# Performance work log

Hardware: AMD Instinct MI355X
Metric: run time of the kernel (lower is better)

Reference implementation:

```python
import jax, jax.numpy as jnp
import numpy as np

LN_EPS = 1e-3

def setup_inputs() -> dict:
    key = jax.random.key(0)
    ks = jax.random.split(key, 3)
    B, H, W, C = 32, 64, 48, 256
    groups = 8
    d = C // groups
    x = jax.random.normal(ks[0], (B, H, W, C), dtype=jnp.float32)
    conv1x1_w = jax.random.normal(ks[1], (d, d), dtype=jnp.float32) * (1.0 / np.sqrt(d))
    conv1x1_b = jnp.zeros((d,), dtype=jnp.float32)
    conv3x3_w = jax.random.normal(ks[2], (3, 3, d, d), dtype=jnp.float32) * (1.0 / np.sqrt(9 * d))
    conv3x3_b = jnp.zeros((d,), dtype=jnp.float32)
    ln_gamma = jnp.ones((d,), dtype=jnp.float32)
    ln_beta = jnp.zeros((d,), dtype=jnp.float32)
    return {"x": x, "conv1x1_w": conv1x1_w, "conv1x1_b": conv1x1_b,
            "conv3x3_w": conv3x3_w, "conv3x3_b": conv3x3_b,
            "ln_gamma": ln_gamma, "ln_beta": ln_beta, "groups": groups}


def reference(x, conv1x1_w, conv1x1_b, conv3x3_w, conv3x3_b, ln_gamma, ln_beta, groups):
    B, H, W, C = x.shape
    g = groups
    d = C // g
    # group split: [B,H,W,C] -> [B*g, H, W, d]
    gx = x.reshape(B, H, W, g, d).transpose(0, 3, 1, 2, 4).reshape(B * g, H, W, d)
    # adaptive pools to (H,1) and (1,W) == mean over W / mean over H
    x_h = gx.mean(axis=2, keepdims=True)                 # [Bg,H,1,d]
    x_w = gx.mean(axis=1, keepdims=True)                 # [Bg,1,W,d]
    hw = jnp.concatenate([x_h, x_w.transpose(0, 2, 1, 3)], axis=1)  # [Bg,H+W,1,d]
    # conv1x1 == per-position linear over channels
    hw = jnp.einsum('bhwd,de->bhwe', hw, conv1x1_w) + conv1x1_b
    xh = jax.nn.sigmoid(hw[:, :H])                       # [Bg,H,1,d]
    xw = jax.nn.sigmoid(hw[:, H:].transpose(0, 2, 1, 3)) # [Bg,1,W,d]
    # LayerNorm over last axis
    y = gx * xh * xw
    mu = y.mean(axis=-1, keepdims=True)
    var = jnp.mean(jnp.square(y - mu), axis=-1, keepdims=True)
    x1 = (y - mu) * jax.lax.rsqrt(var + LN_EPS) * ln_gamma + ln_beta
    # conv3x3 SAME on grouped features
    x2 = jax.lax.conv_general_dilated(
        gx, conv3x3_w, window_strides=(1, 1), padding='SAME',
        dimension_numbers=('NHWC', 'HWIO', 'NHWC')) + conv3x3_b
    # channel softmax of GAP, cross matmuls -> spatial gate
    x11 = jax.nn.softmax(x1.mean(axis=(1, 2)), axis=-1)  # [Bg,d]
    x21 = jax.nn.softmax(x2.mean(axis=(1, 2)), axis=-1)  # [Bg,d]
    w1 = jnp.einsum('bd,bhwd->bhw', x11, x2)
    w2 = jnp.einsum('bd,bhwd->bhw', x21, x1)
    gate = jax.nn.sigmoid((w1 + w2)[..., None])          # [Bg,H,W,1]
    out = gx * gate
    out = out.reshape(B, g, H, W, d).transpose(0, 2, 3, 1, 4).reshape(B, H, W, C)
    return out
```

## Files before the change

### kernel.cpp

```cpp
#include <hip/hip_runtime.h>
#include <math.h>

#define B_ 32
#define H_ 64
#define W_ 48
#define C_ 256
#define G_ 8
#define D_ 32
#define BG_ (B_*G_)
#define LN_EPS_ 1e-3f
#define NPIX_ (H_*W_)
#define XROWB 3072

typedef short bf16x8 __attribute__((ext_vector_type(8)));
typedef float f32x4 __attribute__((ext_vector_type(4)));

__device__ __forceinline__ float sigmoidf_(float v) { return 1.0f / (1.0f + expf(-v)); }

__device__ __forceinline__ unsigned short f2bf(float f) {
    unsigned u = __float_as_uint(f);
    u = u + 0x7fffu + ((u >> 16) & 1u);
    return (unsigned short)(u >> 16);
}
__device__ __forceinline__ float bflo(unsigned u) { return __uint_as_float(u << 16); }
__device__ __forceinline__ float bfhi(unsigned u) { return __uint_as_float(u & 0xffff0000u); }

__device__ __forceinline__ int swz16(int px, int slot) {
    return ((px << 6) + (slot << 4)) ^ ((px & 7) << 4);
}

__global__ __launch_bounds__(256) void k0_prep(const float* __restrict__ w3,
                                               unsigned short* __restrict__ wbf)
{
    int i = blockIdx.x * 256 + threadIdx.x;
    if (i < 9 * D_ * D_) {
        int t = i >> 10;
        int rem = i & 1023;
        int e = rem >> 5, d = rem & 31;
        wbf[i] = f2bf(w3[((t << 5) + d) * D_ + e]);
    }
}

__global__ __launch_bounds__(512) void k1_means(const float* __restrict__ x,
                                                const float* __restrict__ w1,
                                                const float* __restrict__ b1,
                                                unsigned short* __restrict__ xbf,
                                                unsigned short* __restrict__ xhb,
                                                unsigned short* __restrict__ xwb)
{
    __shared__ float mh[H_][D_];
    __shared__ float mwp[8][W_][D_];
    __shared__ float wls[D_ * D_];
    int bg = blockIdx.x;
    int b = bg >> 3, gi = bg & 7;
    const float* base = x + (size_t)b * H_ * W_ * C_ + gi * D_;
    int t = threadIdx.x;
    int lane = t & 63;
    int wv = t >> 6;
    int c4 = lane & 7;
    int pxg = lane >> 3;

    for (int i = t; i < D_ * D_; i += 512) wls[i] = w1[i];

    float4 colp[6];
    #pragma unroll
    for (int j = 0; j < 6; ++j) colp[j] = make_float4(0.f, 0.f, 0.f, 0.f);

    for (int i = 0; i < 8; i += 2) {
        int ha = (wv << 3) + i;
        int hb = ha + 1;
        const float* rowa = base + (size_t)ha * W_ * C_;
        const float* rowb = base + (size_t)hb * W_ * C_;
        float4 va[6], vb[6];
        #pragma unroll
        for (int j = 0; j < 6; ++j) {
            va[j] = *(const float4*)(rowa + (size_t)(pxg + 8 * j) * C_ + (c4 << 2));
            vb[j] = *(const float4*)(rowb + (size_t)(pxg + 8 * j) * C_ + (c4 << 2));
        }
        char* xrowa = (char*)xbf + (((size_t)bg << 6) + ha) * XROWB;
        char* xrowb = (char*)xbf + (((size_t)bg << 6) + hb) * XROWB;
        float4 rpa = make_float4(0.f, 0.f, 0.f, 0.f);
        float4 rpb = make_float4(0.f, 0.f, 0.f, 0.f);
        #pragma unroll
        for (int j = 0; j < 6; ++j) {
            int px = pxg + 8 * j;
            int addr = (((px << 6) + (c4 << 3))) ^ ((px & 7) << 4);
            float4 v = va[j];
            unsigned u0 = (unsigned)f2bf(v.x) | ((unsigned)f2bf(v.y) << 16);
            unsigned u1 = (unsigned)f2bf(v.z) | ((unsigned)f2bf(v.w) << 16);
            *(uint2*)(xrowa + addr) = make_uint2(u0, u1);
            colp[j].x += v.x; colp[j].y += v.y; colp[j].z += v.z; colp[j].w += v.w;
            rpa.x += v.x; rpa.y += v.y; rpa.z += v.z; rpa.w += v.w;
            float4 u = vb[j];
            unsigned w0 = (unsigned)f2bf(u.x) | ((unsigned)f2bf(u.y) << 16);
            unsigned w1_ = (unsigned)f2bf(u.z) | ((unsigned)f2bf(u.w) << 16);
            *(uint2*)(xrowb + addr) = make_uint2(w0, w1_);
            colp[j].x += u.x; colp[j].y += u.y; colp[j].z += u.z; colp[j].w += u.w;
            rpb.x += u.x; rpb.y += u.y; rpb.z += u.z; rpb.w += u.w;
        }
        #pragma unroll
        for (int s = 8; s <= 32; s <<= 1) {
            rpa.x += __shfl_xor(rpa.x, s); rpa.y += __shfl_xor(rpa.y, s);
            rpa.z += __shfl_xor(rpa.z, s); rpa.w += __shfl_xor(rpa.w, s);
            rpb.x += __shfl_xor(rpb.x, s); rpb.y += __shfl_xor(rpb.y, s);
            rpb.z += __shfl_xor(rpb.z, s); rpb.w += __shfl_xor(rpb.w, s);
        }
        if (lane < 8) {
            *(float4*)&mh[ha][c4 << 2] = rpa;
            *(float4*)&mh[hb][c4 << 2] = rpb;
        }
    }
    #pragma unroll
    for (int j = 0; j < 6; ++j)
        *(float4*)&mwp[wv][pxg + 8 * j][c4 << 2] = colp[j];
    __syncthreads();

    for (int i = t; i < W_ * D_; i += 512) {
        int px = i >> 5, c = i & 31;
        float s = 0.f;
        #pragma unroll
        for (int v = 0; v < 8; ++v) s += mwp[v][px][c];
        mwp[0][px][c] = s;
    }
    __syncthreads();

    for (int i = t; i < (H_ + W_) * D_; i += 512) {
        int pos = i >> 5, e = i & 31;
        const float* m = (pos < H_) ? mh[pos] : mwp[0][pos - H_];
        float scale = (pos < H_) ? (1.0f / W_) : (1.0f / H_);
        float dot = 0.f;
        #pragma unroll
        for (int d = 0; d < D_; ++d) dot += m[d] * wls[d * D_ + e];
        unsigned short s = f2bf(sigmoidf_(b1[e] + dot * scale));
        if (pos < H_) xhb[(((size_t)bg << 6) + pos) * D_ + e] = s;
        else          xwb[((size_t)bg * W_ + (pos - H_)) * D_ + e] = s;
    }
}

__global__ __launch_bounds__(256, 4) void k3_conv(const unsigned short* __restrict__ xbf,
                                                  const unsigned short* __restrict__ wbf,
                                                  const float* __restrict__ b3,
                                                  const unsigned short* __restrict__ xhb,
                                                  const unsigned short* __restrict__ xwb,
                                                  const float* __restrict__ gamma,
                                                  const float* __restrict__ beta,
                                                  unsigned short* __restrict__ x2,
                                                  float* __restrict__ s1,
                                                  float* __restrict__ s2)
{
    __shared__ unsigned short sbuf[10 * W_ * D_];
    int d = blockIdx.x;
    int k = d >> 3;
    int bg = (d & 7) + ((k & 31) << 3);
    int h0 = (k >> 5) << 3;
    int t = threadIdx.x;
    int lane = t & 63;
    int wv = t >> 6;

    const int e0 = lane & 15;
    const int ko = (lane >> 4) << 3;
    bf16x8 wf[9][2];
    #pragma unroll
    for (int tp = 0; tp < 9; ++tp)
        #pragma unroll
        for (int n = 0; n < 2; ++n)
            wf[tp][n] = *(const bf16x8*)(const void*)(wbf + (((tp << 5) + (n << 4) + e0) << 5) + ko);
    float be0 = b3[e0], be1 = b3[e0 + 16];

    int sA = (h0 == 0) ? 1 : 0;
    int sB = (h0 == 56) ? 8 : 9;
    const char* src = (const char*)xbf + (((size_t)bg << 6) + (h0 - 1 + sA)) * XROWB;
    char* ldsb = (char*)sbuf + sA * XROWB;
    int nch = (sB - sA + 1) * 3;
    for (int ch = wv; ch < nch; ch += 4) {
        __builtin_amdgcn_global_load_lds(
            (const __attribute__((address_space(1))) unsigned*)(const void*)(src + (ch << 10) + (lane << 4)),
            (__attribute__((address_space(3))) unsigned*)(void*)(ldsb + (ch << 10)),
            16, 0, 0);
    }
    if (h0 == 0 && t < 192)  *(uint4*)((char*)sbuf + (t << 4)) = make_uint4(0, 0, 0, 0);
    if (h0 == 56 && t < 192) *(uint4*)((char*)sbuf + 9 * XROWB + (t << 4)) = make_uint4(0, 0, 0, 0);
    __syncthreads();

    int swz9[9]; bool inv9[9];
    #pragma unroll
    for (int m = 0; m < 3; ++m)
        #pragma unroll
        for (int dw = 0; dw < 3; ++dw) {
            int pxi = (m << 4) + (lane & 15) + dw - 1;
            int pxc = pxi < 0 ? 0 : (pxi > 47 ? 47 : pxi);
            swz9[m * 3 + dw] = swz16(pxc, lane >> 4);
            inv9[m * 3 + dw] = (pxi != pxc);
        }
    const bf16x8 z8 = {0, 0, 0, 0, 0, 0, 0, 0};

    float s2p0 = 0.f, s2p1 = 0.f;
    for (int q = 0; q < 2; ++q) {
        int r = (wv << 1) + q;
        int h = h0 + r;
        #pragma unroll
        for (int m = 0; m < 3; ++m) {
            int w0 = m << 4;
            f32x4 acc0 = {be0, be0, be0, be0};
            f32x4 acc1 = {be1, be1, be1, be1};
            #pragma unroll
            for (int dh = 0; dh < 3; ++dh) {
                int srowB = (r + dh) * XROWB;
                #pragma unroll
                for (int dw = 0; dw < 3; ++dw) {
                    bf16x8 a = *(const bf16x8*)(const void*)((const char*)sbuf + srowB + swz9[m * 3 + dw]);
                    if ((m == 0 && dw == 0) || (m == 2 && dw == 2)) {
                        if (inv9[m * 3 + dw]) a = z8;
                    }
                    acc0 = __builtin_amdgcn_mfma_f32_16x16x32_bf16(a, wf[dh * 3 + dw][0], acc0, 0, 0, 0);
                    acc1 = __builtin_amdgcn_mfma_f32_16x16x32_bf16(a, wf[dh * 3 + dw][1], acc1, 0, 0, 0);
                }
            }
            #pragma unroll
            for (int rg = 0; rg < 4; ++rg) {
                int pw = w0 + ((lane >> 4) << 2) + rg;
                size_t off = (((size_t)bg * H_ + h) * W_ + pw) * D_;
                x2[off + e0]      = f2bf(acc0[rg]);
                x2[off + e0 + 16] = f2bf(acc1[rg]);
                s2p0 += acc0[rg];
                s2p1 += acc1[rg];
            }
        }
    }
    s2p0 += __shfl_xor(s2p0, 16); s2p0 += __shfl_xor(s2p0, 32);
    s2p1 += __shfl_xor(s2p1, 16); s2p1 += __shfl_xor(s2p1, 32);
    if (lane < 16) {
        atomicAdd(&s2[bg * D_ + e0], s2p0);
        atomicAdd(&s2[bg * D_ + e0 + 16], s2p1);
    }

    float s1p[32];
    #pragma unroll
    for (int c = 0; c < 32; ++c) s1p[c] = 0.f;
    for (int pl = t; pl < 8 * W_; pl += 256) {
        int r = pl / W_;
        int w = pl - r * W_;
        int srowB = (r + 1) * XROWB;
        const uint4* ph4 = (const uint4*)(xhb + (((size_t)bg << 6) + h0 + r) * D_);
        const uint4* pw4 = (const uint4*)(xwb + ((size_t)bg * W_ + w) * D_);
        float y[32];
        float mu = 0.f;
        #pragma unroll
        for (int j = 0; j < 4; ++j) {
            uint4 uv = *(const uint4*)((const char*)sbuf + srowB + swz16(w, j));
            uint4 uh = ph4[j];
            uint4 uw = pw4[j];
            float vv[8], ah[8], aw[8];
            vv[0]=bflo(uv.x); vv[1]=bfhi(uv.x); vv[2]=bflo(uv.y); vv[3]=bfhi(uv.y);
            vv[4]=bflo(uv.z); vv[5]=bfhi(uv.z); vv[6]=bflo(uv.w); vv[7]=bfhi(uv.w);
            ah[0]=bflo(uh.x); ah[1]=bfhi(uh.x); ah[2]=bflo(uh.y); ah[3]=bfhi(uh.y);
            ah[4]=bflo(uh.z); ah[5]=bfhi(uh.z); ah[6]=bflo(uh.w); ah[7]=bfhi(uh.w);
            aw[0]=bflo(uw.x); aw[1]=bfhi(uw.x); aw[2]=bflo(uw.y); aw[3]=bfhi(uw.y);
            aw[4]=bflo(uw.z); aw[5]=bfhi(uw.z); aw[6]=bflo(uw.w); aw[7]=bfhi(uw.w);
            #pragma unroll
            for (int kk = 0; kk < 8; ++kk) {
                float yy = vv[kk] * ah[kk] * aw[kk];
                y[j * 8 + kk] = yy;
                mu += yy;
            }
        }
        mu *= (1.0f / D_);
        float var = 0.f;
        #pragma unroll
        for (int c = 0; c < 32; ++c) { float dl = y[c] - mu; var += dl * dl; }
        var *= (1.0f / D_);
        float rs = rsqrtf(var + LN_EPS_);
        #pragma unroll
        for (int c4 = 0; c4 < 8; ++c4) {
            float4 gq = ((const float4*)gamma)[c4];
            float4 bt = ((const float4*)beta)[c4];
            s1p[4 * c4 + 0] += (y[4 * c4 + 0] - mu) * rs * gq.x + bt.x;
            s1p[4 * c4 + 1] += (y[4 * c4 + 1] - mu) * rs * gq.y + bt.y;
            s1p[4 * c4 + 2] += (y[4 * c4 + 2] - mu) * rs * gq.z + bt.z;
            s1p[4 * c4 + 3] += (y[4 * c4 + 3] - mu) * rs * gq.w + bt.w;
        }
    }
    #pragma unroll
    for (int c = 0; c < 32; ++c) {
        float vv = s1p[c];
        vv += __shfl_xor(vv, 1);  vv += __shfl_xor(vv, 2);  vv += __shfl_xor(vv, 4);
        vv += __shfl_xor(vv, 8);  vv += __shfl_xor(vv, 16); vv += __shfl_xor(vv, 32);
        s1p[c] = vv;
    }
    if (lane == 0) {
        #pragma unroll
        for (int c = 0; c < 32; ++c) atomicAdd(&s1[bg * D_ + c], s1p[c]);
    }
}

__global__ __launch_bounds__(64) void k4_softmax(const float* __restrict__ s1,
                                                 const float* __restrict__ s2,
                                                 float* __restrict__ x11,
                                                 float* __restrict__ x21)
{
    int bg = blockIdx.x;
    int lane = threadIdx.x;
    const float* s = (lane < 32) ? s1 : s2;
    float* o = (lane < 32) ? x11 : x21;
    int c = lane & 31;
    float v = s[bg * D_ + c] * (1.0f / (float)NPIX_);
    float m = v;
    m = fmaxf(m, __shfl_xor(m, 1));  m = fmaxf(m, __shfl_xor(m, 2));
    m = fmaxf(m, __shfl_xor(m, 4));  m = fmaxf(m, __shfl_xor(m, 8));
    m = fmaxf(m, __shfl_xor(m, 16));
    float e = expf(v - m);
    float sm = e;
    sm += __shfl_xor(sm, 1);  sm += __shfl_xor(sm, 2);
    sm += __shfl_xor(sm, 4);  sm += __shfl_xor(sm, 8);
    sm += __shfl_xor(sm, 16);
    o[bg * D_ + c] = e / sm;
}

__global__ __launch_bounds__(192) void k5_final(const unsigned short* __restrict__ xbf,
                                                const unsigned short* __restrict__ xhb,
                                                const unsigned short* __restrict__ xwb,
                                                const float* __restrict__ gamma,
                                                const float* __restrict__ beta,
                                                const unsigned short* __restrict__ x2,
                                                const float* __restrict__ x11,
                                                const float* __restrict__ x21,
                                                float* __restrict__ out)
{
    int d = blockIdx.x;
    int k = d >> 3;
    int bg = (d & 7) + ((k & 31) << 3);
    int h0 = (k >> 5) << 2;
    int tid = threadIdx.x;
    int r = tid / W_;
    int w = tid % W_;
    int h = h0 + r;
    int b = bg >> 3, gi = bg & 7;

    const char* xrow = (const char*)xbf + (((size_t)bg << 6) + h) * XROWB;
    const uint4* ph4 = (const uint4*)(xhb + (((size_t)bg << 6) + h) * D_);
    const uint4* pw4 = (const uint4*)(xwb + ((size_t)bg * W_ + w) * D_);

    float v[32], y[32];
    float mu = 0.f;
    #pragma unroll
    for (int j = 0; j < 4; ++j) {
        uint4 uv = *(const uint4*)(xrow + swz16(w, j));
        uint4 uh = ph4[j];
        uint4 uw = pw4[j];
        float ah[8], aw[8];
        v[j*8+0]=bflo(uv.x); v[j*8+1]=bfhi(uv.x); v[j*8+2]=bflo(uv.y); v[j*8+3]=bfhi(uv.y);
        v[j*8+4]=bflo(uv.z); v[j*8+5]=bfhi(uv.z); v[j*8+6]=bflo(uv.w); v[j*8+7]=bfhi(uv.w);
        ah[0]=bflo(uh.x); ah[1]=bfhi(uh.x); ah[2]=bflo(uh.y); ah[3]=bfhi(uh.y);
        ah[4]=bflo(uh.z); ah[5]=bfhi(uh.z); ah[6]=bflo(uh.w); ah[7]=bfhi(uh.w);
        aw[0]=bflo(uw.x); aw[1]=bfhi(uw.x); aw[2]=bflo(uw.y); aw[3]=bfhi(uw.y);
        aw[4]=bflo(uw.z); aw[5]=bfhi(uw.z); aw[6]=bflo(uw.w); aw[7]=bfhi(uw.w);
        #pragma unroll
        for (int kk = 0; kk < 8; ++kk) {
            float yy = v[j * 8 + kk] * ah[kk] * aw[kk];
            y[j * 8 + kk] = yy;
            mu += yy;
        }
    }
    mu *= (1.0f / D_);
    float var = 0.f;
    #pragma unroll
    for (int c = 0; c < D_; ++c) { float dl = y[c] - mu; var += dl * dl; }
    var *= (1.0f / D_);
    float rs = rsqrtf(var + LN_EPS_);

    const uint4* x2q = (const uint4*)(x2 + (((size_t)bg * H_ + h) * W_ + w) * D_);
    float w1 = 0.f, w2 = 0.f;
    #pragma unroll
    for (int j = 0; j < 4; ++j) {
        uint4 u = x2q[j];
        float xv[8];
        xv[0] = bflo(u.x); xv[1] = bfhi(u.x); xv[2] = bflo(u.y); xv[3] = bfhi(u.y);
        xv[4] = bflo(u.z); xv[5] = bfhi(u.z); xv[6] = bflo(u.w); xv[7] = bfhi(u.w);
        #pragma unroll
        for (int kk = 0; kk < 8; ++kk) {
            int c = j * 8 + kk;
            float x1v = (y[c] - mu) * rs * gamma[c] + beta[c];
            w1 += x11[bg * D_ + c] * xv[kk];
            w2 += x21[bg * D_ + c] * x1v;
        }
    }
    float gate = sigmoidf_(w1 + w2);

    size_t pixoff = (size_t)b * H_ * W_ * C_ + ((size_t)h * W_ + w) * C_ + gi * D_;
    float4* op = (float4*)(out + pixoff);
    #pragma unroll
    for (int q = 0; q < 8; ++q) {
        float4 tq;
        tq.x = v[4 * q + 0] * gate; tq.y = v[4 * q + 1] * gate;
        tq.z = v[4 * q + 2] * gate; tq.w = v[4 * q + 3] * gate;
        op[q] = tq;
    }
}

extern "C" void kernel_launch(void* const* d_in, const int* in_sizes, int n_in,
                              void* d_out, int out_size, void* d_ws, size_t ws_size,
                              hipStream_t stream)
{
    const float* x     = (const float*)d_in[0];
    const float* w1    = (const float*)d_in[1];
    const float* b1    = (const float*)d_in[2];
    const float* w3    = (const float*)d_in[3];
    const float* b3    = (const float*)d_in[4];
    const float* gamma = (const float*)d_in[5];
    const float* beta  = (const float*)d_in[6];

    char* wsb = (char*)d_ws;
    unsigned short* x2  = (unsigned short*)wsb;
    unsigned short* xbf = (unsigned short*)(wsb + 50331648);
    unsigned short* xhb = (unsigned short*)(wsb + 100663296);
    unsigned short* xwb = (unsigned short*)(wsb + 101711872);
    float* s1  = (float*)(wsb + 102498304);
    float* s2  = (float*)(wsb + 102531072);
    float* x11 = (float*)(wsb + 102563840);
    float* x21 = (float*)(wsb + 102596608);
    unsigned short* wbf = (unsigned short*)(wsb + 102629376);

    hipMemsetAsync(s1, 0, 65536, stream);

    k0_prep<<<36, 256, 0, stream>>>(w3, wbf);
    k1_means<<<BG_, 512, 0, stream>>>(x, w1, b1, xbf, xhb, xwb);
    k3_conv<<<BG_ * 8, 256, 0, stream>>>(xbf, wbf, b3, xhb, xwb, gamma, beta, x2, s1, s2);
    k4_softmax<<<BG_, 64, 0, stream>>>(s1, s2, x11, x21);
    k5_final<<<BG_ * (H_ / 4), 192, 0, stream>>>(xbf, xhb, xwb, gamma, beta, x2, x11, x21,
                                                 (float*)d_out);
}
```

Baseline: 356.9 us.

## Compute conv3x3 channel means analytically and fuse conv with final gating

The spatial mean of the 3x3 conv output is now derived in closed form from the row/column sums and corner pixels times the conv weights, computed inside the means kernel. This removes the need to materialize x2 and the bf16 copy of x in global memory. The conv is recomputed in the final kernel, which reads fp32 x directly and reduces each conv output against x11 immediately to form the gate term. The means kernel also computes the LayerNorm channel sums itself, which adds a second pass over x with extra per-block work. The s1 memset and atomics are replaced by a block-level reduction.

Measured after the change: 292.6 us. -18.0%, faster.

```diff
diff --git a/kernel.cpp b/kernel.cpp
--- a/kernel.cpp
+++ b/kernel.cpp
@@ -10,7 +10,7 @@
 #define BG_ (B_*G_)
 #define LN_EPS_ 1e-3f
 #define NPIX_ (H_*W_)
-#define XROWB 3072
+#define SROWB 3072
 
 typedef short bf16x8 __attribute__((ext_vector_type(8)));
 typedef float f32x4 __attribute__((ext_vector_type(4)));
@@ -44,13 +44,26 @@
 __global__ __launch_bounds__(512) void k1_means(const float* __restrict__ x,
                                                 const float* __restrict__ w1,
                                                 const float* __restrict__ b1,
-                                                unsigned short* __restrict__ xbf,
+                                                const float* __restrict__ w3,
+                                                const float* __restrict__ b3,
+                                                const float* __restrict__ gamma,
+                                                const float* __restrict__ beta,
                                                 unsigned short* __restrict__ xhb,
-                                                unsigned short* __restrict__ xwb)
+                                                unsigned short* __restrict__ xwb,
+                                                float* __restrict__ s1,
+                                                float* __restrict__ s2)
 {
     __shared__ float mh[H_][D_];
     __shared__ float mwp[8][W_][D_];
     __shared__ float wls[D_ * D_];
+    __shared__ float xhf[H_][D_];
+    __shared__ float xwf[W_][36];
+    __shared__ float cst[4][D_];
+    __shared__ float Tg[D_];
+    __shared__ float Sl[9][D_];
+    __shared__ float S2p[9][D_];
+    __shared__ float s1red[8][D_];
+
     int bg = blockIdx.x;
     int b = bg >> 3, gi = bg & 7;
     const float* base = x + (size_t)b * H_ * W_ * C_ + gi * D_;
@@ -77,24 +90,14 @@
             va[j] = *(const float4*)(rowa + (size_t)(pxg + 8 * j) * C_ + (c4 << 2));
             vb[j] = *(const float4*)(rowb + (size_t)(pxg + 8 * j) * C_ + (c4 << 2));
         }
-        char* xrowa = (char*)xbf + (((size_t)bg << 6) + ha) * XROWB;
-        char* xrowb = (char*)xbf + (((size_t)bg << 6) + hb) * XROWB;
         float4 rpa = make_float4(0.f, 0.f, 0.f, 0.f);
         float4 rpb = make_float4(0.f, 0.f, 0.f, 0.f);
         #pragma unroll
         for (int j = 0; j < 6; ++j) {
-            int px = pxg + 8 * j;
-            int addr = (((px << 6) + (c4 << 3))) ^ ((px & 7) << 4);
             float4 v = va[j];
-            unsigned u0 = (unsigned)f2bf(v.x) | ((unsigned)f2bf(v.y) << 16);
-            unsigned u1 = (unsigned)f2bf(v.z) | ((unsigned)f2bf(v.w) << 16);
-            *(uint2*)(xrowa + addr) = make_uint2(u0, u1);
             colp[j].x += v.x; colp[j].y += v.y; colp[j].z += v.z; colp[j].w += v.w;
             rpa.x += v.x; rpa.y += v.y; rpa.z += v.z; rpa.w += v.w;
             float4 u = vb[j];
-            unsigned w0 = (unsigned)f2bf(u.x) | ((unsigned)f2bf(u.y) << 16);
-            unsigned w1_ = (unsigned)f2bf(u.z) | ((unsigned)f2bf(u.w) << 16);
-            *(uint2*)(xrowb + addr) = make_uint2(w0, w1_);
             colp[j].x += u.x; colp[j].y += u.y; colp[j].z += u.z; colp[j].w += u.w;
             rpb.x += u.x; rpb.y += u.y; rpb.z += u.z; rpb.w += u.w;
         }
@@ -122,8 +125,19 @@
         for (int v = 0; v < 8; ++v) s += mwp[v][px][c];
         mwp[0][px][c] = s;
     }
-    __syncthreads();
-
+    if (t < 128) {
+        int k = t >> 5, c = t & 31;
+        int hh = (k >> 1) ? (H_ - 1) : 0;
+        int ww = (k & 1) ? (W_ - 1) : 0;
+        cst[k][c] = base[(size_t)(hh * W_ + ww) * C_ + c];
+    }
+    __syncthreads();
+
+    if (t < 32) {
+        float s = 0.f;
+        for (int h = 0; h < H_; ++h) s += mh[h][t];
+        Tg[t] = s;
+    }
     for (int i = t; i < (H_ + W_) * D_; i += 512) {
         int pos = i >> 5, e = i & 31;
         const float* m = (pos < H_) ? mh[pos] : mwp[0][pos - H_];
@@ -131,138 +145,60 @@
         float dot = 0.f;
         #pragma unroll
         for (int d = 0; d < D_; ++d) dot += m[d] * wls[d * D_ + e];
-        unsigned short s = f2bf(sigmoidf_(b1[e] + dot * scale));
-        if (pos < H_) xhb[(((size_t)bg << 6) + pos) * D_ + e] = s;
-        else          xwb[((size_t)bg * W_ + (pos - H_)) * D_ + e] = s;
-    }
-}
-
-__global__ __launch_bounds__(256, 4) void k3_conv(const unsigned short* __restrict__ xbf,
-                                                  const unsigned short* __restrict__ wbf,
-                                                  const float* __restrict__ b3,
-                                                  const unsigned short* __restrict__ xhb,
-                                                  const unsigned short* __restrict__ xwb,
-                                                  const float* __restrict__ gamma,
-                                                  const float* __restrict__ beta,
-                                                  unsigned short* __restrict__ x2,
-                                                  float* __restrict__ s1,
-                                                  float* __restrict__ s2)
-{
-    __shared__ unsigned short sbuf[10 * W_ * D_];
-    int d = blockIdx.x;
-    int k = d >> 3;
-    int bg = (d & 7) + ((k & 31) << 3);
-    int h0 = (k >> 5) << 3;
-    int t = threadIdx.x;
-    int lane = t & 63;
-    int wv = t >> 6;
-
-    const int e0 = lane & 15;
-    const int ko = (lane >> 4) << 3;
-    bf16x8 wf[9][2];
-    #pragma unroll
-    for (int tp = 0; tp < 9; ++tp)
-        #pragma unroll
-        for (int n = 0; n < 2; ++n)
-            wf[tp][n] = *(const bf16x8*)(const void*)(wbf + (((tp << 5) + (n << 4) + e0) << 5) + ko);
-    float be0 = b3[e0], be1 = b3[e0 + 16];
-
-    int sA = (h0 == 0) ? 1 : 0;
-    int sB = (h0 == 56) ? 8 : 9;
-    const char* src = (const char*)xbf + (((size_t)bg << 6) + (h0 - 1 + sA)) * XROWB;
-    char* ldsb = (char*)sbuf + sA * XROWB;
-    int nch = (sB - sA + 1) * 3;
-    for (int ch = wv; ch < nch; ch += 4) {
-        __builtin_amdgcn_global_load_lds(
-            (const __attribute__((address_space(1))) unsigned*)(const void*)(src + (ch << 10) + (lane << 4)),
-            (__attribute__((address_space(3))) unsigned*)(void*)(ldsb + (ch << 10)),
-            16, 0, 0);
-    }
-    if (h0 == 0 && t < 192)  *(uint4*)((char*)sbuf + (t << 4)) = make_uint4(0, 0, 0, 0);
-    if (h0 == 56 && t < 192) *(uint4*)((char*)sbuf + 9 * XROWB + (t << 4)) = make_uint4(0, 0, 0, 0);
-    __syncthreads();
-
-    int swz9[9]; bool inv9[9];
-    #pragma unroll
-    for (int m = 0; m < 3; ++m)
-        #pragma unroll
-        for (int dw = 0; dw < 3; ++dw) {
-            int pxi = (m << 4) + (lane & 15) + dw - 1;
-            int pxc = pxi < 0 ? 0 : (pxi > 47 ? 47 : pxi);
-            swz9[m * 3 + dw] = swz16(pxc, lane >> 4);
-            inv9[m * 3 + dw] = (pxi != pxc);
-        }
-    const bf16x8 z8 = {0, 0, 0, 0, 0, 0, 0, 0};
-
-    float s2p0 = 0.f, s2p1 = 0.f;
-    for (int q = 0; q < 2; ++q) {
-        int r = (wv << 1) + q;
-        int h = h0 + r;
-        #pragma unroll
-        for (int m = 0; m < 3; ++m) {
-            int w0 = m << 4;
-            f32x4 acc0 = {be0, be0, be0, be0};
-            f32x4 acc1 = {be1, be1, be1, be1};
-            #pragma unroll
-            for (int dh = 0; dh < 3; ++dh) {
-                int srowB = (r + dh) * XROWB;
-                #pragma unroll
-                for (int dw = 0; dw < 3; ++dw) {
-                    bf16x8 a = *(const bf16x8*)(const void*)((const char*)sbuf + srowB + swz9[m * 3 + dw]);
-                    if ((m == 0 && dw == 0) || (m == 2 && dw == 2)) {
-                        if (inv9[m * 3 + dw]) a = z8;
-                    }
-                    acc0 = __builtin_amdgcn_mfma_f32_16x16x32_bf16(a, wf[dh * 3 + dw][0], acc0, 0, 0, 0);
-                    acc1 = __builtin_amdgcn_mfma_f32_16x16x32_bf16(a, wf[dh * 3 + dw][1], acc1, 0, 0, 0);
-                }
-            }
-            #pragma unroll
-            for (int rg = 0; rg < 4; ++rg) {
-                int pw = w0 + ((lane >> 4) << 2) + rg;
-                size_t off = (((size_t)bg * H_ + h) * W_ + pw) * D_;
-                x2[off + e0]      = f2bf(acc0[rg]);
-                x2[off + e0 + 16] = f2bf(acc1[rg]);
-                s2p0 += acc0[rg];
-                s2p1 += acc1[rg];
-            }
-        }
-    }
-    s2p0 += __shfl_xor(s2p0, 16); s2p0 += __shfl_xor(s2p0, 32);
-    s2p1 += __shfl_xor(s2p1, 16); s2p1 += __shfl_xor(s2p1, 32);
-    if (lane < 16) {
-        atomicAdd(&s2[bg * D_ + e0], s2p0);
-        atomicAdd(&s2[bg * D_ + e0 + 16], s2p1);
+        float sg = sigmoidf_(b1[e] + dot * scale);
+        if (pos < H_) { xhf[pos][e] = sg; xhb[(((size_t)bg << 6) + pos) * D_ + e] = f2bf(sg); }
+        else { xwf[pos - H_][e] = sg; xwb[((size_t)bg * W_ + (pos - H_)) * D_ + e] = f2bf(sg); }
+    }
+    __syncthreads();
+
+    if (t < 288) {
+        int tap = t >> 5, d = t & 31;
+        int dh = tap / 3, dw = tap % 3;
+        float S = Tg[d];
+        if (dh == 0) S -= mh[H_ - 1][d];
+        else if (dh == 2) S -= mh[0][d];
+        if (dw == 0) S -= mwp[0][W_ - 1][d];
+        else if (dw == 2) S -= mwp[0][0][d];
+        if (dh != 1 && dw != 1) S += cst[(dh == 0 ? 2 : 0) + (dw == 0 ? 1 : 0)][d];
+        Sl[tap][d] = S;
+    }
+    __syncthreads();
+    if (t < 288) {
+        int tap = t >> 5, e = t & 31;
+        float a = 0.f;
+        #pragma unroll
+        for (int d = 0; d < D_; ++d) a += w3[((tap << 5) + d) * D_ + e] * Sl[tap][d];
+        S2p[tap][e] = a;
+    }
+    __syncthreads();
+    if (t < 32) {
+        float a = (float)NPIX_ * b3[t];
+        #pragma unroll
+        for (int tap = 0; tap < 9; ++tap) a += S2p[tap][t];
+        s2[bg * D_ + t] = a;
     }
 
     float s1p[32];
     #pragma unroll
     for (int c = 0; c < 32; ++c) s1p[c] = 0.f;
-    for (int pl = t; pl < 8 * W_; pl += 256) {
-        int r = pl / W_;
-        int w = pl - r * W_;
-        int srowB = (r + 1) * XROWB;
-        const uint4* ph4 = (const uint4*)(xhb + (((size_t)bg << 6) + h0 + r) * D_);
-        const uint4* pw4 = (const uint4*)(xwb + ((size_t)bg * W_ + w) * D_);
+    #pragma unroll
+    for (int k = 0; k < 6; ++k) {
+        int p = t + (k << 9);
+        int h = p / W_;
+        int w = p - h * W_;
+        const float4* vp = (const float4*)(base + (size_t)(h * W_ + w) * C_);
         float y[32];
         float mu = 0.f;
         #pragma unroll
-        for (int j = 0; j < 4; ++j) {
-            uint4 uv = *(const uint4*)((const char*)sbuf + srowB + swz16(w, j));
-            uint4 uh = ph4[j];
-            uint4 uw = pw4[j];
-            float vv[8], ah[8], aw[8];
-            vv[0]=bflo(uv.x); vv[1]=bfhi(uv.x); vv[2]=bflo(uv.y); vv[3]=bfhi(uv.y);
-            vv[4]=bflo(uv.z); vv[5]=bfhi(uv.z); vv[6]=bflo(uv.w); vv[7]=bfhi(uv.w);
-            ah[0]=bflo(uh.x); ah[1]=bfhi(uh.x); ah[2]=bflo(uh.y); ah[3]=bfhi(uh.y);
-            ah[4]=bflo(uh.z); ah[5]=bfhi(uh.z); ah[6]=bflo(uh.w); ah[7]=bfhi(uh.w);
-            aw[0]=bflo(uw.x); aw[1]=bfhi(uw.x); aw[2]=bflo(uw.y); aw[3]=bfhi(uw.y);
-            aw[4]=bflo(uw.z); aw[5]=bfhi(uw.z); aw[6]=bflo(uw.w); aw[7]=bfhi(uw.w);
-            #pragma unroll
-            for (int kk = 0; kk < 8; ++kk) {
-                float yy = vv[kk] * ah[kk] * aw[kk];
-                y[j * 8 + kk] = yy;
-                mu += yy;
-            }
+        for (int j = 0; j < 8; ++j) {
+            float4 v = vp[j];
+            float4 a = *(const float4*)&xhf[h][j << 2];
+            float4 bw = *(const float4*)&xwf[w][j << 2];
+            y[4 * j + 0] = v.x * a.x * bw.x;
+            y[4 * j + 1] = v.y * a.y * bw.y;
+            y[4 * j + 2] = v.z * a.z * bw.z;
+            y[4 * j + 3] = v.w * a.w * bw.w;
+            mu += y[4 * j + 0] + y[4 * j + 1] + y[4 * j + 2] + y[4 * j + 3];
         }
         mu *= (1.0f / D_);
         float var = 0.f;
@@ -271,13 +207,13 @@
         var *= (1.0f / D_);
         float rs = rsqrtf(var + LN_EPS_);
         #pragma unroll
-        for (int c4 = 0; c4 < 8; ++c4) {
-            float4 gq = ((const float4*)gamma)[c4];
-            float4 bt = ((const float4*)beta)[c4];
-            s1p[4 * c4 + 0] += (y[4 * c4 + 0] - mu) * rs * gq.x + bt.x;
-            s1p[4 * c4 + 1] += (y[4 * c4 + 1] - mu) * rs * gq.y + bt.y;
-            s1p[4 * c4 + 2] += (y[4 * c4 + 2] - mu) * rs * gq.z + bt.z;
-            s1p[4 * c4 + 3] += (y[4 * c4 + 3] - mu) * rs * gq.w + bt.w;
+        for (int j = 0; j < 8; ++j) {
+            float4 gq = ((const float4*)gamma)[j];
+            float4 bt = ((const float4*)beta)[j];
+            s1p[4 * j + 0] += (y[4 * j + 0] - mu) * rs * gq.x + bt.x;
+            s1p[4 * j + 1] += (y[4 * j + 1] - mu) * rs * gq.y + bt.y;
+            s1p[4 * j + 2] += (y[4 * j + 2] - mu) * rs * gq.z + bt.z;
+            s1p[4 * j + 3] += (y[4 * j + 3] - mu) * rs * gq.w + bt.w;
         }
     }
     #pragma unroll
@@ -289,7 +225,14 @@
     }
     if (lane == 0) {
         #pragma unroll
-        for (int c = 0; c < 32; ++c) atomicAdd(&s1[bg * D_ + c], s1p[c]);
+        for (int c = 0; c < 32; ++c) s1red[wv][c] = s1p[c];
+    }
+    __syncthreads();
+    if (t < 32) {
+        float a = 0.f;
+        #pragma unroll
+        for (int v = 0; v < 8; ++v) a += s1red[v][t];
+        s1[bg * D_ + t] = a;
     }
 }
 
@@ -316,84 +259,152 @@
     o[bg * D_ + c] = e / sm;
 }
 
-__global__ __launch_bounds__(192) void k5_final(const unsigned short* __restrict__ xbf,
-                                                const unsigned short* __restrict__ xhb,
-                                                const unsigned short* __restrict__ xwb,
-                                                const float* __restrict__ gamma,
-                                                const float* __restrict__ beta,
-                                                const unsigned short* __restrict__ x2,
-                                                const float* __restrict__ x11,
-                                                const float* __restrict__ x21,
-                                                float* __restrict__ out)
+__global__ __launch_bounds__(256) void k5_conv(const float* __restrict__ x,
+                                               const unsigned short* __restrict__ wbf,
+                                               const float* __restrict__ b3,
+                                               const unsigned short* __restrict__ xhb,
+                                               const unsigned short* __restrict__ xwb,
+                                               const float* __restrict__ gamma,
+                                               const float* __restrict__ beta,
+                                               const float* __restrict__ x11,
+                                               const float* __restrict__ x21,
+                                               float* __restrict__ out)
 {
-    int d = blockIdx.x;
-    int k = d >> 3;
-    int bg = (d & 7) + ((k & 31) << 3);
-    int h0 = (k >> 5) << 2;
-    int tid = threadIdx.x;
-    int r = tid / W_;
-    int w = tid % W_;
-    int h = h0 + r;
+    __shared__ unsigned short sbuf[10 * W_ * D_];
+    __shared__ float wbuf[8][W_];
+    int bi = blockIdx.x;
+    int bg = bi >> 3;
+    int h0 = (bi & 7) << 3;
     int b = bg >> 3, gi = bg & 7;
-
-    const char* xrow = (const char*)xbf + (((size_t)bg << 6) + h) * XROWB;
-    const uint4* ph4 = (const uint4*)(xhb + (((size_t)bg << 6) + h) * D_);
-    const uint4* pw4 = (const uint4*)(xwb + ((size_t)bg * W_ + w) * D_);
-
-    float v[32], y[32];
-    float mu = 0.f;
-    #pragma unroll
-    for (int j = 0; j < 4; ++j) {
-        uint4 uv = *(const uint4*)(xrow + swz16(w, j));
-        uint4 uh = ph4[j];
-        uint4 uw = pw4[j];
-        float ah[8], aw[8];
-        v[j*8+0]=bflo(uv.x); v[j*8+1]=bfhi(uv.x); v[j*8+2]=bflo(uv.y); v[j*8+3]=bfhi(uv.y);
-        v[j*8+4]=bflo(uv.z); v[j*8+5]=bfhi(uv.z); v[j*8+6]=bflo(uv.w); v[j*8+7]=bfhi(uv.w);
-        ah[0]=bflo(uh.x); ah[1]=bfhi(uh.x); ah[2]=bflo(uh.y); ah[3]=bfhi(uh.y);
-        ah[4]=bflo(uh.z); ah[5]=bfhi(uh.z); ah[6]=bflo(uh.w); ah[7]=bfhi(uh.w);
-        aw[0]=bflo(uw.x); aw[1]=bfhi(uw.x); aw[2]=bflo(uw.y); aw[3]=bfhi(uw.y);
-        aw[4]=bflo(uw.z); aw[5]=bfhi(uw.z); aw[6]=bflo(uw.w); aw[7]=bfhi(uw.w);
-        #pragma unroll
-        for (int kk = 0; kk < 8; ++kk) {
-            float yy = v[j * 8 + kk] * ah[kk] * aw[kk];
-            y[j * 8 + kk] = yy;
-            mu += yy;
-        }
-    }
-    mu *= (1.0f / D_);
-    float var = 0.f;
-    #pragma unroll
-    for (int c = 0; c < D_; ++c) { float dl = y[c] - mu; var += dl * dl; }
-    var *= (1.0f / D_);
-    float rs = rsqrtf(var + LN_EPS_);
-
-    const uint4* x2q = (const uint4*)(x2 + (((size_t)bg * H_ + h) * W_ + w) * D_);
-    float w1 = 0.f, w2 = 0.f;
-    #pragma unroll
-    for (int j = 0; j < 4; ++j) {
-        uint4 u = x2q[j];
-        float xv[8];
-        xv[0] = bflo(u.x); xv[1] = bfhi(u.x); xv[2] = bflo(u.y); xv[3] = bfhi(u.y);
-        xv[4] = bflo(u.z); xv[5] = bfhi(u.z); xv[6] = bflo(u.w); xv[7] = bfhi(u.w);
-        #pragma unroll
-        for (int kk = 0; kk < 8; ++kk) {
-            int c = j * 8 + kk;
+    const float* base = x + (size_t)b * H_ * W_ * C_ + gi * D_;
+    int t = threadIdx.x;
+    int lane = t & 63;
+    int wv = t >> 6;
+    const int e0 = lane & 15;
+    const int ko = (lane >> 4) << 3;
+
+    bf16x8 wf[9][2];
+    #pragma unroll
+    for (int tp = 0; tp < 9; ++tp)
+        #pragma unroll
+        for (int n = 0; n < 2; ++n)
+            wf[tp][n] = *(const bf16x8*)(const void*)(wbf + (((tp << 5) + (n << 4) + e0) << 5) + ko);
+    float be0 = b3[e0], be1 = b3[e0 + 16];
+    float a110 = x11[bg * D_ + e0], a111 = x11[bg * D_ + e0 + 16];
+
+    #pragma unroll
+    for (int kk = 0; kk < 15; ++kk) {
+        int i = t + (kk << 8);
+        int r = i / 384;
+        int rem = i - r * 384;
+        int w = rem >> 3, cc = rem & 7;
+        int hh = h0 - 1 + r;
+        unsigned u0 = 0, u1 = 0;
+        if (hh >= 0 && hh < H_) {
+            float4 v = *(const float4*)(base + (size_t)(hh * W_ + w) * C_ + (cc << 2));
+            u0 = (unsigned)f2bf(v.x) | ((unsigned)f2bf(v.y) << 16);
+            u1 = (unsigned)f2bf(v.z) | ((unsigned)f2bf(v.w) << 16);
+        }
+        int addr = r * SROWB + ((((w << 6) + (cc << 3))) ^ ((w & 7) << 4));
+        *(uint2*)((char*)sbuf + addr) = make_uint2(u0, u1);
+    }
+    __syncthreads();
+
+    int swz9[9]; bool inv9[9];
+    #pragma unroll
+    for (int m = 0; m < 3; ++m)
+        #pragma unroll
+        for (int dw = 0; dw < 3; ++dw) {
+            int pxi = (m << 4) + e0 + dw - 1;
+            int pxc = pxi < 0 ? 0 : (pxi > 47 ? 47 : pxi);
+            swz9[m * 3 + dw] = swz16(pxc, lane >> 4);
+            inv9[m * 3 + dw] = (pxi != pxc);
+        }
+    const bf16x8 z8 = {0, 0, 0, 0, 0, 0, 0, 0};
+
+    for (int q = 0; q < 2; ++q) {
+        int r = (wv << 1) + q;
+        #pragma unroll
+        for (int m = 0; m < 3; ++m) {
+            f32x4 acc0 = {be0, be0, be0, be0};
+            f32x4 acc1 = {be1, be1, be1, be1};
+            #pragma unroll
+            for (int dh = 0; dh < 3; ++dh) {
+                int srowB = (r + dh) * SROWB;
+                #pragma unroll
+                for (int dw = 0; dw < 3; ++dw) {
+                    bf16x8 a = *(const bf16x8*)(const void*)((const char*)sbuf + srowB + swz9[m * 3 + dw]);
+                    if ((m == 0 && dw == 0) || (m == 2 && dw == 2)) {
+                        if (inv9[m * 3 + dw]) a = z8;
+                    }
+                    acc0 = __builtin_amdgcn_mfma_f32_16x16x32_bf16(a, wf[dh * 3 + dw][0], acc0, 0, 0, 0);
+                    acc1 = __builtin_amdgcn_mfma_f32_16x16x32_bf16(a, wf[dh * 3 + dw][1], acc1, 0, 0, 0);
+                }
+            }
+            #pragma unroll
+            for (int rg = 0; rg < 4; ++rg) {
+                float p = a110 * acc0[rg] + a111 * acc1[rg];
+                p += __shfl_xor(p, 1); p += __shfl_xor(p, 2);
+                p += __shfl_xor(p, 4); p += __shfl_xor(p, 8);
+                if (e0 == 0) wbuf[r][(m << 4) + ((lane >> 4) << 2) + rg] = p;
+            }
+        }
+    }
+    __syncthreads();
+
+    for (int p = t; p < 8 * W_; p += 256) {
+        int r = p / W_;
+        int w = p - r * W_;
+        int h = h0 + r;
+        int srowB = (r + 1) * SROWB;
+        const uint4* ph4 = (const uint4*)(xhb + (((size_t)bg << 6) + h) * D_);
+        const uint4* pw4 = (const uint4*)(xwb + ((size_t)bg * W_ + w) * D_);
+        float y[32];
+        float mu = 0.f;
+        #pragma unroll
+        for (int j = 0; j < 4; ++j) {
+            uint4 uv = *(const uint4*)((const char*)sbuf + srowB + swz16(w, j));
+            uint4 uh = ph4[j];
+            uint4 uw = pw4[j];
+            float vv[8], ah[8], aw[8];
+            vv[0]=bflo(uv.x); vv[1]=bfhi(uv.x); vv[2]=bflo(uv.y); vv[3]=bfhi(uv.y);
+            vv[4]=bflo(uv.z); vv[5]=bfhi(uv.z); vv[6]=bflo(uv.w); vv[7]=bfhi(uv.w);
+            ah[0]=bflo(uh.x); ah[1]=bfhi(uh.x); ah[2]=bflo(uh.y); ah[3]=bfhi(uh.y);
+            ah[4]=bflo(uh.z); ah[5]=bfhi(uh.z); ah[6]=bflo(uh.w); ah[7]=bfhi(uh.w);
+            aw[0]=bflo(uw.x); aw[1]=bfhi(uw.x); aw[2]=bflo(uw.y); aw[3]=bfhi(uw.y);
+            aw[4]=bflo(uw.z); aw[5]=bfhi(uw.z); aw[6]=bflo(uw.w); aw[7]=bfhi(uw.w);
+            #pragma unroll
+            for (int kk = 0; kk < 8; ++kk) {
+                float yy = vv[kk] * ah[kk] * aw[kk];
+                y[j * 8 + kk] = yy;
+                mu += yy;
+            }
+        }
+        mu *= (1.0f / D_);
+        float var = 0.f;
+        #pragma unroll
+        for (int c = 0; c < D_; ++c) { float dl = y[c] - mu; var += dl * dl; }
+        var *= (1.0f / D_);
+        float rs = rsqrtf(var + LN_EPS_);
+
+        float w2 = 0.f;
+        #pragma unroll
+        for (int c = 0; c < D_; ++c) {
             float x1v = (y[c] - mu) * rs * gamma[c] + beta[c];
-            w1 += x11[bg * D_ + c] * xv[kk];
             w2 += x21[bg * D_ + c] * x1v;
         }
-    }
-    float gate = sigmoidf_(w1 + w2);
-
-    size_t pixoff = (size_t)b * H_ * W_ * C_ + ((size_t)h * W_ + w) * C_ + gi * D_;
-    float4* op = (float4*)(out + pixoff);
-    #pragma unroll
-    for (int q = 0; q < 8; ++q) {
-        float4 tq;
-        tq.x = v[4 * q + 0] * gate; tq.y = v[4 * q + 1] * gate;
-        tq.z = v[4 * q + 2] * gate; tq.w = v[4 * q + 3] * gate;
-        op[q] = tq;
+        float gate = sigmoidf_(wbuf[r][w] + w2);
+
+        const float4* vp = (const float4*)(base + (size_t)(h * W_ + w) * C_);
+        float4* op = (float4*)(out + (size_t)b * H_ * W_ * C_ + (size_t)(h * W_ + w) * C_ + gi * D_);
+        #pragma unroll
+        for (int j = 0; j < 8; ++j) {
+            float4 vv = vp[j];
+            float4 tq;
+            tq.x = vv.x * gate; tq.y = vv.y * gate;
+            tq.z = vv.z * gate; tq.w = vv.w * gate;
+            op[j] = tq;
+        }
     }
 }
 
@@ -410,22 +421,17 @@
     const float* beta  = (const float*)d_in[6];
 
     char* wsb = (char*)d_ws;
-    unsigned short* x2  = (unsigned short*)wsb;
-    unsigned short* xbf = (unsigned short*)(wsb + 50331648);
-    unsigned short* xhb = (unsigned short*)(wsb + 100663296);
-    unsigned short* xwb = (unsigned short*)(wsb + 101711872);
-    float* s1  = (float*)(wsb + 102498304);
-    float* s2  = (float*)(wsb + 102531072);
-    float* x11 = (float*)(wsb + 102563840);
-    float* x21 = (float*)(wsb + 102596608);
-    unsigned short* wbf = (unsigned short*)(wsb + 102629376);
-
-    hipMemsetAsync(s1, 0, 65536, stream);
+    unsigned short* xhb = (unsigned short*)wsb;
+    unsigned short* xwb = (unsigned short*)(wsb + 1048576);
+    float* s1  = (float*)(wsb + 1835008);
+    float* s2  = (float*)(wsb + 1867776);
+    float* x11 = (float*)(wsb + 1900544);
+    float* x21 = (float*)(wsb + 1933312);
+    unsigned short* wbf = (unsigned short*)(wsb + 1966080);
 
     k0_prep<<<36, 256, 0, stream>>>(w3, wbf);
-    k1_means<<<BG_, 512, 0, stream>>>(x, w1, b1, xbf, xhb, xwb);
-    k3_conv<<<BG_ * 8, 256, 0, stream>>>(xbf, wbf, b3, xhb, xwb, gamma, beta, x2, s1, s2);
+    k1_means<<<BG_, 512, 0, stream>>>(x, w1, b1, w3, b3, gamma, beta, xhb, xwb, s1, s2);
     k4_softmax<<<BG_, 64, 0, stream>>>(s1, s2, x11, x21);
-    k5_final<<<BG_ * (H_ / 4), 192, 0, stream>>>(xbf, xhb, xwb, gamma, beta, x2, x11, x21,
-                                                 (float*)d_out);
-}
+    k5_conv<<<BG_ * 8, 256, 0, stream>>>(x, wbf, b3, xhb, xwb, gamma, beta, x11, x21,
+                                         (float*)d_out);
+}
```
